# Optimization experiments

Hardware: AMD Instinct MI355X
Metric: run time of the kernel (lower is better)

Reference implementation:

```python
import jax, jax.numpy as jnp
import numpy as np

ITER_ROUTING = 3
FINAL_LAMBDA = 0.01
EPS = 1e-9

N = 4
CHILD_SPACE = 12
KERNEL = 3
STRIDE = 1
CHILD_CAPS = 16
PARENT_CAPS = 32
POSE = 16


def _routing_map(child_space, k, s):
    # (child_space^2, parent_space^2) binary map: child c feeds parent p.
    parent_space = (child_space - k) // s + 1
    m = np.zeros((child_space * child_space, parent_space * parent_space), np.float32)
    for pr in range(parent_space):
        for pc in range(parent_space):
            p = pr * parent_space + pc
            for r in range(k):
                for c in range(k):
                    m[(pr * s + r) * child_space + (pc * s + c), p] = 1.0
    return m


def setup_inputs() -> dict:
    key = jax.random.key(0)
    k1, k2, k3, k4 = jax.random.split(key, 4)
    parent_space = (CHILD_SPACE - KERNEL) // STRIDE + 1
    kk = KERNEL * KERNEL
    votes = jax.random.normal(k1, (N * parent_space * parent_space, kk * CHILD_CAPS, PARENT_CAPS, POSE), jnp.float32)
    acts = jax.random.uniform(k2, (N * parent_space * parent_space, kk * CHILD_CAPS, 1), dtype=jnp.float32)
    beta_v = jax.random.normal(k3, (1, 1, 1, 1, PARENT_CAPS, 1), jnp.float32)
    beta_a = jax.random.normal(k4, (1, 1, 1, 1, PARENT_CAPS, 1), jnp.float32)
    srm = jnp.asarray(_routing_map(CHILD_SPACE, KERNEL, STRIDE))
    return {"votes_ij": votes, "activations_i": acts, "beta_v": beta_v, "beta_a": beta_a,
            "spatial_routing_matrix": srm, "batch_size": N, "kk": kk}


def _em_routing(votes_ij, activations_i, beta_v, beta_a, srm, batch_size, kk):
    Nb = batch_size
    C2, P2 = srm.shape  # child_space^2, parent_space^2
    P = int(round(P2 ** 0.5))
    K_total, O, ch = votes_ij.shape[1], votes_ij.shape[2], votes_ij.shape[3]
    child_caps = K_total // kk

    votes = votes_ij.reshape(Nb, P, P, K_total, O, ch)
    act_i = activations_i.reshape(Nb, P, P, K_total, 1, 1)

    # children per parent, ascending child index (stable argsort on -1/0 values)
    cidx = jnp.argsort(-srm, axis=0)[:kk].T           # (P2, kk)
    seg = cidx.reshape(-1)                            # (P2*kk,) child id per (parent, slot)
    ppc = jnp.sum(srm, axis=1)                        # parents-per-child, (C2,)
    # init_rr: 1 / (parents_per_child * parent_caps + 1e-9), gathered per parent slot
    rr0 = (1.0 / (ppc[cidx] * O + 1e-9)).reshape(1, P, P, kk, 1, 1)
    rr = jnp.broadcast_to(rr0, (1, P, P, kk, child_caps, O)).reshape(1, P, P, K_total, O, 1)

    layer_norm_factor = 100.0 / (float(K_total) / float(O))

    def m_step(rr, it):
        lam = FINAL_LAMBDA * (1.0 - 0.95 ** (it + 1))
        rr_prime = rr * act_i                                            # (N,P,P,K,O,1)
        rr_prime_sum = jnp.sum(rr_prime, axis=-3, keepdims=True)         # (N,P,P,1,O,1)
        mean_j = jnp.sum(rr_prime * votes, axis=-3, keepdims=True) / (rr_prime_sum + EPS)
        var_j = jnp.sum(rr_prime * jnp.square(votes - mean_j), axis=-3, keepdims=True) / (rr_prime_sum + EPS)
        cost_j_h = (beta_v + 0.5 * jnp.log(var_j + EPS)) * rr_prime_sum * layer_norm_factor
        cost_j = jnp.sum(cost_j_h, axis=-1, keepdims=True)               # (N,P,P,1,O,1)
        cost_mean = jnp.mean(cost_j, axis=-2, keepdims=True)
        cost_stdv = jnp.sqrt(jnp.sum(jnp.square(cost_j - cost_mean), axis=-2, keepdims=True) / O)
        act_j = jax.nn.sigmoid(lam * (beta_a + (cost_mean - cost_j) / (cost_stdv + EPS)))
        return act_j, mean_j, var_j

    def e_step(act_j, mean_j, var_j):
        # log N(vote; mean_j, var_j) per parent + log activation
        o_p0 = -jnp.sum(jnp.square(votes - mean_j) / (2.0 * var_j), axis=-1, keepdims=True)
        o_p2 = -0.5 * jnp.sum(jnp.log(2.0 * np.pi * var_j), axis=-1, keepdims=True)
        zz = jnp.log(act_j + EPS) + o_p0 + o_p2                          # (N,P,P,K,O,1)
        # softmax over ALL parents of each child (spatial kk slots x parent_caps),
        # done via segment reductions keyed by child id (== sparse/softmax/dense of original)
        z = jnp.moveaxis(zz.reshape(Nb, P2 * kk, child_caps, O), 1, 0)   # (P2*kk, N, cc, O)
        m = jax.ops.segment_max(jnp.max(z, axis=-1), seg, num_segments=C2)  # (C2, N, cc)
        m = jnp.where(jnp.isinf(m), 0.0, m)
        e = jnp.exp(z - m[seg][..., None])
        denom = jax.ops.segment_sum(jnp.sum(e, axis=-1), seg, num_segments=C2)
        rr_new = e / denom[seg][..., None]
        return jnp.moveaxis(rr_new, 0, 1).reshape(Nb, P, P, K_total, O, 1)

    for it in range(ITER_ROUTING):
        act_j, mean_j, var_j = m_step(rr, it)
        if it < ITER_ROUTING - 1:
            rr = e_step(act_j, mean_j, var_j)

    poses_j = mean_j[:, :, :, 0]        # (N,P,P,O,16)
    activations_j = act_j[:, :, :, 0]   # (N,P,P,O,1)
    return poses_j, activations_j


def reference(votes_ij, activations_i, beta_v, beta_a, spatial_routing_matrix, batch_size, kk):
    return _em_routing(votes_ij, activations_i, beta_v, beta_a, spatial_routing_matrix, batch_size, kk)
```

## Files before the change

kernel.cpp:

```cpp
#include <hip/hip_runtime.h>
#include <hip/hip_fp16.h>
#include <math.h>

#define NB     4
#define P      10
#define P2     100
#define CS     12
#define CCAPS  16
#define KTOT   144
#define O      32
#define POSE   16
#define VSZ    73728
#define EPSF   1e-9f
#define LNF    22.2222222222222222f
#define TWO_PI 6.28318530717958647f
#define NBP    400
#define NKQ    3
#define KPU    48
#define SUNITS (NBP*NKQ)
#define EUNITS (NB*CS*CS*2)

#define LAM0 0.0005f
#define LAM1 0.000975f
#define LAM2 0.00142625f

__device__ float g_rr [NBP*KTOT*O];
__device__ float g_zz [NBP*KTOT*O];
__device__ float g_m1 [SUNITS*512];
__device__ float g_m2 [SUNITS*512];
__device__ float g_sv [SUNITS*O];

__device__ __forceinline__ int npar(int x) {
    int a = x + 1, b = CS - x;
    int m = a < 3 ? a : 3;
    return m < b ? m : b;
}

__device__ __forceinline__ void up8(uint4 u, float* f) {
    float2 a = __half22float2(*(__half2*)&u.x);
    float2 b = __half22float2(*(__half2*)&u.y);
    float2 c = __half22float2(*(__half2*)&u.z);
    float2 d = __half22float2(*(__half2*)&u.w);
    f[0] = a.x; f[1] = a.y; f[2] = b.x; f[3] = b.y;
    f[4] = c.x; f[5] = c.y; f[6] = d.x; f[7] = d.y;
}

__global__ __launch_bounds__(256)
void v_kernel(const float* __restrict__ votes, const float* __restrict__ acts,
              __half* __restrict__ hv)
{
    __shared__ float actl[KPU];
    __shared__ __align__(16) float rrp[KPU*O];
    __shared__ float4 lm1[256];
    __shared__ float4 lm2[256];
    __shared__ float  lss[256];

    const int tid = threadIdx.x;
    const int u   = blockIdx.x;
    const int bp  = u / NKQ;
    const int kq  = u - bp * NKQ;
    const int k0  = kq * KPU;
    const int ks  = tid >> 7;
    const int q   = tid & 127;
    const int o   = q >> 2;

    if (tid < KPU) actl[tid] = acts[bp * KTOT + k0 + tid];
    __syncthreads();

    for (int f = tid; f < KPU * O / 4; f += 256) {
        int kl = f >> 3;
        int kg = k0 + kl, kslot = kg >> 4;
        int kr = kslot / 3, kc = kslot - kr * 3;
        int p = bp % P2, pr = p / P, pc = p - pr * P;
        float ppc = (float)(npar(pr + kr) * npar(pc + kc));
        float r = actl[kl] / (ppc * 32.0f + EPSF);
        ((float4*)rrp)[f] = make_float4(r, r, r, r);
    }
    __syncthreads();

    const float* vb  = votes + (size_t)bp * VSZ + (size_t)(k0 + ks * 24) * 512 + q * 4;
    __half*      hb  = hv    + (size_t)bp * VSZ + (size_t)(k0 + ks * 24) * 512 + q * 4;
    const float* rr0 = rrp + (ks * 24) * O + o;
    float  s  = 0.f;
    float4 m1 = make_float4(0.f, 0.f, 0.f, 0.f);
    float4 m2 = make_float4(0.f, 0.f, 0.f, 0.f);
    #pragma unroll 8
    for (int i = 0; i < 24; ++i) {
        float  rp = rr0[i * O];
        float4 v  = *(const float4*)(vb + i * 512);
        s += rp;
        m1.x += rp * v.x;       m1.y += rp * v.y;
        m1.z += rp * v.z;       m1.w += rp * v.w;
        m2.x += rp * v.x * v.x; m2.y += rp * v.y * v.y;
        m2.z += rp * v.z * v.z; m2.w += rp * v.w * v.w;
        __half2 ha = __floats2half2_rn(v.x, v.y);
        __half2 hbv = __floats2half2_rn(v.z, v.w);
        uint2 st;
        st.x = *(unsigned int*)&ha;
        st.y = *(unsigned int*)&hbv;
        *(uint2*)(hb + i * 512) = st;
    }
    lm1[tid] = m1; lm2[tid] = m2; lss[tid] = s;
    __syncthreads();

    if (tid < 128) {
        float4 a = lm1[tid], b = lm1[tid + 128];
        m1 = make_float4(a.x + b.x, a.y + b.y, a.z + b.z, a.w + b.w);
        a = lm2[tid]; b = lm2[tid + 128];
        m2 = make_float4(a.x + b.x, a.y + b.y, a.z + b.z, a.w + b.w);
        s = lss[tid] + lss[tid + 128];
        ((float4*)g_m1)[u * 128 + tid] = m1;
        ((float4*)g_m2)[u * 128 + tid] = m2;
        if ((tid & 3) == 0) g_sv[u * O + (tid >> 2)] = s;
    }
}

__global__ __launch_bounds__(256)
void s16_kernel(const __half* __restrict__ hv, const float* __restrict__ acts)
{
    __shared__ float actl[KPU];
    __shared__ __align__(16) float rrp[KPU*O];
    __shared__ float4 lm1[512];
    __shared__ float4 lm2[512];
    __shared__ float  lss[256];

    const int tid = threadIdx.x;
    const int u   = blockIdx.x;
    const int bp  = u / NKQ;
    const int kq  = u - bp * NKQ;
    const int k0  = kq * KPU;
    const int ks  = tid >> 6;
    const int qp  = tid & 63;
    const int o   = qp >> 1;

    if (tid < KPU) actl[tid] = acts[bp * KTOT + k0 + tid];
    __syncthreads();

    for (int f = tid; f < KPU * O / 4; f += 256) {
        int kl = f >> 3;
        float4 r4 = ((const float4*)(g_rr + (size_t)bp * (KTOT * O) + k0 * O))[f];
        float a = actl[kl];
        r4.x *= a; r4.y *= a; r4.z *= a; r4.w *= a;
        ((float4*)rrp)[f] = r4;
    }
    __syncthreads();

    const __half* vb = hv + (size_t)bp * VSZ + (size_t)(k0 + ks * 12) * 512 + qp * 8;
    const float* rr0 = rrp + (ks * 12) * O + o;
    float s = 0.f;
    float m1[8], m2[8];
    #pragma unroll
    for (int j = 0; j < 8; ++j) { m1[j] = 0.f; m2[j] = 0.f; }
    #pragma unroll 4
    for (int i = 0; i < 12; ++i) {
        float rp = rr0[i * O];
        uint4 u4 = *(const uint4*)(vb + i * 512);
        float f[8]; up8(u4, f);
        s += rp;
        #pragma unroll
        for (int j = 0; j < 8; ++j) {
            m1[j] += rp * f[j];
            m2[j] += rp * f[j] * f[j];
        }
    }
    lm1[tid*2]   = make_float4(m1[0], m1[1], m1[2], m1[3]);
    lm1[tid*2+1] = make_float4(m1[4], m1[5], m1[6], m1[7]);
    lm2[tid*2]   = make_float4(m2[0], m2[1], m2[2], m2[3]);
    lm2[tid*2+1] = make_float4(m2[4], m2[5], m2[6], m2[7]);
    lss[tid] = s;
    __syncthreads();

    if (tid < 64) {
        #pragma unroll
        for (int j = 0; j < 2; ++j) {
            float4 a0 = lm1[(tid)*2+j],       a1 = lm1[(64+tid)*2+j];
            float4 a2 = lm1[(128+tid)*2+j],   a3 = lm1[(192+tid)*2+j];
            float4 r = make_float4(a0.x+a1.x+a2.x+a3.x, a0.y+a1.y+a2.y+a3.y,
                                   a0.z+a1.z+a2.z+a3.z, a0.w+a1.w+a2.w+a3.w);
            ((float4*)g_m1)[u * 128 + tid*2 + j] = r;
            float4 b0 = lm2[(tid)*2+j],       b1 = lm2[(64+tid)*2+j];
            float4 b2 = lm2[(128+tid)*2+j],   b3 = lm2[(192+tid)*2+j];
            float4 r2 = make_float4(b0.x+b1.x+b2.x+b3.x, b0.y+b1.y+b2.y+b3.y,
                                    b0.z+b1.z+b2.z+b3.z, b0.w+b1.w+b2.w+b3.w);
            ((float4*)g_m2)[u * 128 + tid*2 + j] = r2;
        }
        float sr = lss[tid] + lss[64+tid] + lss[128+tid] + lss[192+tid];
        if ((tid & 1) == 0) g_sv[u * O + (tid >> 1)] = sr;
    }
}

__device__ __forceinline__ void finish_bp(int bp, int tid, float lam,
                                          const float* __restrict__ beta_v,
                                          const float* __restrict__ beta_a,
                                          float4& mean, float4& i2,
                                          float& aj, float& lv2out,
                                          float* costl )
{
    const int o = tid >> 2, c4 = tid & 3;
    float4 m1 = make_float4(0.f, 0.f, 0.f, 0.f);
    float4 m2 = make_float4(0.f, 0.f, 0.f, 0.f);
    float  s  = 0.f;
    #pragma unroll
    for (int j = 0; j < NKQ; ++j) {
        float4 a = ((const float4*)g_m1)[(bp * NKQ + j) * 128 + tid];
        float4 b = ((const float4*)g_m2)[(bp * NKQ + j) * 128 + tid];
        m1.x += a.x; m1.y += a.y; m1.z += a.z; m1.w += a.w;
        m2.x += b.x; m2.y += b.y; m2.z += b.z; m2.w += b.w;
        s += g_sv[(bp * NKQ + j) * O + o];
    }
    float denom = s + EPSF;
    mean = make_float4(m1.x / denom, m1.y / denom, m1.z / denom, m1.w / denom);
    float4 var;
    var.x = fmaxf(m2.x / denom - mean.x * mean.x, 1e-30f);
    var.y = fmaxf(m2.y / denom - mean.y * mean.y, 1e-30f);
    var.z = fmaxf(m2.z / denom - mean.z * mean.z, 1e-30f);
    var.w = fmaxf(m2.w / denom - mean.w * mean.w, 1e-30f);
    i2 = make_float4(0.5f / var.x, 0.5f / var.y, 0.5f / var.z, 0.5f / var.w);
    float lve = logf(var.x + EPSF) + logf(var.y + EPSF)
              + logf(var.z + EPSF) + logf(var.w + EPSF);
    float lv2 = logf(TWO_PI * var.x) + logf(TWO_PI * var.y)
              + logf(TWO_PI * var.z) + logf(TWO_PI * var.w);
    lve += __shfl_xor(lve, 1); lve += __shfl_xor(lve, 2);
    lv2 += __shfl_xor(lv2, 1); lv2 += __shfl_xor(lv2, 2);
    lv2out = lv2;
    if (c4 == 0) costl[o] = (16.f * beta_v[o] + 0.5f * lve) * s * LNF;
    __syncthreads();
    float cm = 0.f;
    #pragma unroll
    for (int i = 0; i < O; ++i) cm += costl[i];
    cm *= (1.f / 32.f);
    float sq = 0.f;
    #pragma unroll
    for (int i = 0; i < O; ++i) { float d = costl[i] - cm; sq += d * d; }
    float cstd = sqrtf(sq * (1.f / 32.f));
    aj = 1.f / (1.f + expf(-lam * (beta_a[o] + (cm - costl[o]) / (cstd + EPSF))));
}

__global__ __launch_bounds__(256)
void zf16_kernel(const __half* __restrict__ hv,
                 const float* __restrict__ beta_v,
                 const float* __restrict__ beta_a, float lam)
{
    __shared__ float4 ml[128];
    __shared__ float4 il[128];
    __shared__ float  zl[O];
    __shared__ float  costl[O];
    __shared__ __align__(16) float zzl[KPU*O];

    const int tid = threadIdx.x;
    const int u   = blockIdx.x;
    const int bp  = u / NKQ;
    const int kq  = u - bp * NKQ;
    const int k0  = kq * KPU;
    const int ks  = tid >> 6;
    const int qp  = tid & 63;
    const int o   = qp >> 1;
    const int h   = qp & 1;

    {
        float4 mean, i2; float aj, lv2;
        if (tid < 128) {
            finish_bp(bp, tid, lam, beta_v, beta_a, mean, i2, aj, lv2, costl);
            ml[tid] = mean; il[tid] = i2;
            if ((tid & 3) == 0)
                zl[tid >> 2] = logf(aj + EPSF) - 0.5f * lv2;
        } else {
            __syncthreads();
        }
    }
    __syncthreads();

    const __half* vb = hv + (size_t)bp * VSZ + (size_t)(k0 + ks * 12) * 512 + qp * 8;
    float4 mA = ml[o*4 + h*2], mB = ml[o*4 + h*2 + 1];
    float4 iA = il[o*4 + h*2], iB = il[o*4 + h*2 + 1];
    float  zp = zl[o];
    #pragma unroll 4
    for (int i = 0; i < 12; ++i) {
        uint4 u4 = *(const uint4*)(vb + i * 512);
        float f[8]; up8(u4, f);
        float d0 = f[0]-mA.x, d1 = f[1]-mA.y, d2 = f[2]-mA.z, d3 = f[3]-mA.w;
        float d4 = f[4]-mB.x, d5 = f[5]-mB.y, d6 = f[6]-mB.z, d7 = f[7]-mB.w;
        float t = d0*d0*iA.x + d1*d1*iA.y + d2*d2*iA.z + d3*d3*iA.w
                + d4*d4*iB.x + d5*d5*iB.y + d6*d6*iB.z + d7*d7*iB.w;
        t += __shfl_xor(t, 1);
        if (h == 0) zzl[(ks * 12 + i) * O + o] = zp - t;
    }
    __syncthreads();
    float4* dst = (float4*)(g_zz + (size_t)bp * (KTOT * O) + k0 * O);
    for (int f = tid; f < KPU * O / 4; f += 256)
        dst[f] = ((float4*)zzl)[f];
}

__global__ __launch_bounds__(256)
void f_last_kernel(const float* __restrict__ beta_v,
                   const float* __restrict__ beta_a,
                   float* __restrict__ out, float lam)
{
    __shared__ float costl[O];
    const int tid = threadIdx.x;
    const int bp  = blockIdx.x;
    float4 mean, i2; float aj, lv2;
    if (tid < 128) {
        finish_bp(bp, tid, lam, beta_v, beta_a, mean, i2, aj, lv2, costl);
        ((float4*)out)[bp * 128 + tid] = mean;
        if ((tid & 3) == 0)
            out[(size_t)NBP * 512 + bp * O + (tid >> 2)] = aj;
    } else {
        __syncthreads();
    }
}

__global__ __launch_bounds__(256)
void e_kernel()
{
    const int tid = threadIdx.x;
    const int u   = blockIdx.x;
    const int b   = u / (CS * CS * 2);
    int r = u - b * (CS * CS * 2);
    const int child = r >> 1, half = r & 1;
    const int cr = child / CS, cl = child - cr * CS;
    const int cc = half * 8 + (tid >> 5), o = tid & 31;

    float zz[9];
    float vmax = -1e30f;
    #pragma unroll
    for (int kr = 0; kr < 3; ++kr) {
        int pr_ = cr - kr;
        #pragma unroll
        for (int kc = 0; kc < 3; ++kc) {
            int pc_ = cl - kc, si = kr * 3 + kc;
            float z = -1e30f;
            if (pr_ >= 0 && pr_ < P && pc_ >= 0 && pc_ < P) {
                int bpp = b * P2 + pr_ * P + pc_;
                z = g_zz[(size_t)bpp * (KTOT * O) + (si * CCAPS + cc) * O + o];
            }
            zz[si] = z;
            vmax = fmaxf(vmax, z);
        }
    }
    vmax = fmaxf(vmax, __shfl_xor(vmax, 1));
    vmax = fmaxf(vmax, __shfl_xor(vmax, 2));
    vmax = fmaxf(vmax, __shfl_xor(vmax, 4));
    vmax = fmaxf(vmax, __shfl_xor(vmax, 8));
    vmax = fmaxf(vmax, __shfl_xor(vmax, 16));

    float ps = 0.f;
    #pragma unroll
    for (int si = 0; si < 9; ++si) {
        float e = (zz[si] > -1e29f) ? expf(zz[si] - vmax) : 0.f;
        zz[si] = e;
        ps += e;
    }
    ps += __shfl_xor(ps, 1);
    ps += __shfl_xor(ps, 2);
    ps += __shfl_xor(ps, 4);
    ps += __shfl_xor(ps, 8);
    ps += __shfl_xor(ps, 16);
    float inv = 1.f / ps;

    #pragma unroll
    for (int kr = 0; kr < 3; ++kr) {
        int pr_ = cr - kr;
        #pragma unroll
        for (int kc = 0; kc < 3; ++kc) {
            int pc_ = cl - kc, si = kr * 3 + kc;
            if (pr_ >= 0 && pr_ < P && pc_ >= 0 && pc_ < P) {
                int bpp = b * P2 + pr_ * P + pc_;
                g_rr[(size_t)bpp * (KTOT * O) + (si * CCAPS + cc) * O + o] = zz[si] * inv;
            }
        }
    }
}

extern "C" void kernel_launch(void* const* d_in, const int* in_sizes, int n_in,
                              void* d_out, int out_size, void* d_ws, size_t ws_size,
                              hipStream_t stream)
{
    (void)in_sizes; (void)n_in; (void)out_size; (void)ws_size;

    const float* votes = (const float*)d_in[0];
    const float* acts  = (const float*)d_in[1];
    const float* bv    = (const float*)d_in[2];
    const float* ba    = (const float*)d_in[3];
    float* out = (float*)d_out;
    __half* hv = (__half*)d_ws;

    dim3 t(256);
    v_kernel<<<dim3(SUNITS), t, 0, stream>>>(votes, acts, hv);
    zf16_kernel<<<dim3(SUNITS), t, 0, stream>>>(hv, bv, ba, LAM0);
    e_kernel<<<dim3(EUNITS), t, 0, stream>>>();

    s16_kernel<<<dim3(SUNITS), t, 0, stream>>>(hv, acts);
    zf16_kernel<<<dim3(SUNITS), t, 0, stream>>>(hv, bv, ba, LAM1);
    e_kernel<<<dim3(EUNITS), t, 0, stream>>>();

    s16_kernel<<<dim3(SUNITS), t, 0, stream>>>(hv, acts);
    f_last_kernel<<<dim3(NBP), t, 0, stream>>>(bv, ba, out, LAM2);
}
```

Before: 257.5 us.

## Fuse softmax e-step into s16 m-step kernel and prefetch votes into registers

```diff
diff --git a/kernel.cpp b/kernel.cpp
--- a/kernel.cpp
+++ b/kernel.cpp
@@ -18,13 +18,11 @@
 #define NKQ    3
 #define KPU    48
 #define SUNITS (NBP*NKQ)
-#define EUNITS (NB*CS*CS*2)
 
 #define LAM0 0.0005f
 #define LAM1 0.000975f
 #define LAM2 0.00142625f
 
-__device__ float g_rr [NBP*KTOT*O];
 __device__ float g_zz [NBP*KTOT*O];
 __device__ float g_m1 [SUNITS*512];
 __device__ float g_m2 [SUNITS*512];
@@ -93,7 +91,7 @@
         m1.z += rp * v.z;       m1.w += rp * v.w;
         m2.x += rp * v.x * v.x; m2.y += rp * v.y * v.y;
         m2.z += rp * v.z * v.z; m2.w += rp * v.w * v.w;
-        __half2 ha = __floats2half2_rn(v.x, v.y);
+        __half2 ha  = __floats2half2_rn(v.x, v.y);
         __half2 hbv = __floats2half2_rn(v.z, v.w);
         uint2 st;
         st.x = *(unsigned int*)&ha;
@@ -115,14 +113,63 @@
     }
 }
 
+__device__ __forceinline__ void finish_bp(int bp, int tid, float lam,
+                                          const float* __restrict__ beta_v,
+                                          const float* __restrict__ beta_a,
+                                          float4& mean, float4& i2,
+                                          float& aj, float& lv2out,
+                                          float* costl )
+{
+    const int o = tid >> 2, c4 = tid & 3;
+    float4 m1 = make_float4(0.f, 0.f, 0.f, 0.f);
+    float4 m2 = make_float4(0.f, 0.f, 0.f, 0.f);
+    float  s  = 0.f;
+    #pragma unroll
+    for (int j = 0; j < NKQ; ++j) {
+        float4 a = ((const float4*)g_m1)[(bp * NKQ + j) * 128 + tid];
+        float4 b = ((const float4*)g_m2)[(bp * NKQ + j) * 128 + tid];
+        m1.x += a.x; m1.y += a.y; m1.z += a.z; m1.w += a.w;
+        m2.x += b.x; m2.y += b.y; m2.z += b.z; m2.w += b.w;
+        s += g_sv[(bp * NKQ + j) * O + o];
+    }
+    float denom = s + EPSF;
+    mean = make_float4(m1.x / denom, m1.y / denom, m1.z / denom, m1.w / denom);
+    float4 var;
+    var.x = fmaxf(m2.x / denom - mean.x * mean.x, 1e-30f);
+    var.y = fmaxf(m2.y / denom - mean.y * mean.y, 1e-30f);
+    var.z = fmaxf(m2.z / denom - mean.z * mean.z, 1e-30f);
+    var.w = fmaxf(m2.w / denom - mean.w * mean.w, 1e-30f);
+    i2 = make_float4(0.5f / var.x, 0.5f / var.y, 0.5f / var.z, 0.5f / var.w);
+    float lve = logf(var.x + EPSF) + logf(var.y + EPSF)
+              + logf(var.z + EPSF) + logf(var.w + EPSF);
+    float lv2 = logf(TWO_PI * var.x) + logf(TWO_PI * var.y)
+              + logf(TWO_PI * var.z) + logf(TWO_PI * var.w);
+    lve += __shfl_xor(lve, 1); lve += __shfl_xor(lve, 2);
+    lv2 += __shfl_xor(lv2, 1); lv2 += __shfl_xor(lv2, 2);
+    lv2out = lv2;
+    if (c4 == 0) costl[o] = (16.f * beta_v[o] + 0.5f * lve) * s * LNF;
+    __syncthreads();
+    float cm = 0.f;
+    #pragma unroll
+    for (int i = 0; i < O; ++i) cm += costl[i];
+    cm *= (1.f / 32.f);
+    float sq = 0.f;
+    #pragma unroll
+    for (int i = 0; i < O; ++i) { float d = costl[i] - cm; sq += d * d; }
+    float cstd = sqrtf(sq * (1.f / 32.f));
+    aj = 1.f / (1.f + expf(-lam * (beta_a[o] + (cm - costl[o]) / (cstd + EPSF))));
+}
+
 __global__ __launch_bounds__(256)
-void s16_kernel(const __half* __restrict__ hv, const float* __restrict__ acts)
-{
-    __shared__ float actl[KPU];
-    __shared__ __align__(16) float rrp[KPU*O];
-    __shared__ float4 lm1[512];
-    __shared__ float4 lm2[512];
-    __shared__ float  lss[256];
+void zf16_kernel(const __half* __restrict__ hv,
+                 const float* __restrict__ beta_v,
+                 const float* __restrict__ beta_a, float lam)
+{
+    __shared__ float4 ml[128];
+    __shared__ float4 il[128];
+    __shared__ float  zl[O];
+    __shared__ float  costl[O];
+    __shared__ __align__(16) float zzl[KPU*O];
 
     const int tid = threadIdx.x;
     const int u   = blockIdx.x;
@@ -132,30 +179,127 @@
     const int ks  = tid >> 6;
     const int qp  = tid & 63;
     const int o   = qp >> 1;
-
-    if (tid < KPU) actl[tid] = acts[bp * KTOT + k0 + tid];
-    __syncthreads();
-
-    for (int f = tid; f < KPU * O / 4; f += 256) {
-        int kl = f >> 3;
-        float4 r4 = ((const float4*)(g_rr + (size_t)bp * (KTOT * O) + k0 * O))[f];
-        float a = actl[kl];
-        r4.x *= a; r4.y *= a; r4.z *= a; r4.w *= a;
-        ((float4*)rrp)[f] = r4;
-    }
-    __syncthreads();
+    const int h   = qp & 1;
 
     const __half* vb = hv + (size_t)bp * VSZ + (size_t)(k0 + ks * 12) * 512 + qp * 8;
-    const float* rr0 = rrp + (ks * 12) * O + o;
+    uint4 vv[12];
+    #pragma unroll
+    for (int i = 0; i < 12; ++i) vv[i] = *(const uint4*)(vb + i * 512);
+
+    {
+        float4 mean, i2; float aj, lv2;
+        if (tid < 128) {
+            finish_bp(bp, tid, lam, beta_v, beta_a, mean, i2, aj, lv2, costl);
+            ml[tid] = mean; il[tid] = i2;
+            if ((tid & 3) == 0)
+                zl[tid >> 2] = logf(aj + EPSF) - 0.5f * lv2;
+        } else {
+            __syncthreads();
+        }
+    }
+    __syncthreads();
+
+    float4 mA = ml[o*4 + h*2], mB = ml[o*4 + h*2 + 1];
+    float4 iA = il[o*4 + h*2], iB = il[o*4 + h*2 + 1];
+    float  zp = zl[o];
+    #pragma unroll
+    for (int i = 0; i < 12; ++i) {
+        float f[8]; up8(vv[i], f);
+        float d0 = f[0]-mA.x, d1 = f[1]-mA.y, d2 = f[2]-mA.z, d3 = f[3]-mA.w;
+        float d4 = f[4]-mB.x, d5 = f[5]-mB.y, d6 = f[6]-mB.z, d7 = f[7]-mB.w;
+        float t = d0*d0*iA.x + d1*d1*iA.y + d2*d2*iA.z + d3*d3*iA.w
+                + d4*d4*iB.x + d5*d5*iB.y + d6*d6*iB.z + d7*d7*iB.w;
+        t += __shfl_xor(t, 1);
+        if (h == 0) zzl[(ks * 12 + i) * O + o] = zp - t;
+    }
+    __syncthreads();
+    float4* dst = (float4*)(g_zz + (size_t)bp * (KTOT * O) + k0 * O);
+    for (int f = tid; f < KPU * O / 4; f += 256)
+        dst[f] = ((float4*)zzl)[f];
+}
+
+__global__ __launch_bounds__(256)
+void se16_kernel(const __half* __restrict__ hv, const float* __restrict__ acts)
+{
+    __shared__ __align__(16) float rrp[KPU*O];
+    __shared__ float4 lm1[512];
+    __shared__ float4 lm2[512];
+    __shared__ float  lss[256];
+
+    const int tid = threadIdx.x;
+    const int u   = blockIdx.x;
+    const int bp  = u / NKQ;
+    const int kq  = u - bp * NKQ;
+    const int k0  = kq * KPU;
+    const int p   = bp % P2;
+    const int b   = bp / P2;
+    const int pr  = p / P, pc = p - pr * P;
+
+    const int ks  = tid >> 6;
+    const int qp  = tid & 63;
+    const int o_s = qp >> 1;
+
+    const __half* vb = hv + (size_t)bp * VSZ + (size_t)(k0 + ks * 12) * 512 + qp * 8;
+    uint4 vv[12];
+    #pragma unroll
+    for (int i = 0; i < 12; ++i) vv[i] = *(const uint4*)(vb + i * 512);
+
+    const int ccl = tid >> 5;
+    const int o   = tid & 31;
+    const int cr  = pr + kq;
+
+    #pragma unroll
+    for (int ci = 0; ci < 3; ++ci) {
+        const int cl = pc + ci;
+        #pragma unroll
+        for (int ccp = 0; ccp < 2; ++ccp) {
+            const int cc = ccl + 8 * ccp;
+            float zv[9];
+            float vmax = -1e30f;
+            #pragma unroll
+            for (int sip = 0; sip < 9; ++sip) {
+                const int krp = sip / 3, kcp = sip - krp * 3;
+                const int pr2 = cr - krp, pc2 = cl - kcp;
+                float z = -1e30f;
+                if (pr2 >= 0 && pr2 < P && pc2 >= 0 && pc2 < P) {
+                    const int bp2 = b * P2 + pr2 * P + pc2;
+                    z = g_zz[(size_t)bp2 * (KTOT * O) + (sip * CCAPS + cc) * O + o];
+                }
+                zv[sip] = z;
+                vmax = fmaxf(vmax, z);
+            }
+            vmax = fmaxf(vmax, __shfl_xor(vmax, 1));
+            vmax = fmaxf(vmax, __shfl_xor(vmax, 2));
+            vmax = fmaxf(vmax, __shfl_xor(vmax, 4));
+            vmax = fmaxf(vmax, __shfl_xor(vmax, 8));
+            vmax = fmaxf(vmax, __shfl_xor(vmax, 16));
+            float ps = 0.f;
+            #pragma unroll
+            for (int sip = 0; sip < 9; ++sip)
+                ps += (zv[sip] > -1e29f) ? expf(zv[sip] - vmax) : 0.f;
+            ps += __shfl_xor(ps, 1);
+            ps += __shfl_xor(ps, 2);
+            ps += __shfl_xor(ps, 4);
+            ps += __shfl_xor(ps, 8);
+            ps += __shfl_xor(ps, 16);
+            const float inv = 1.f / ps;
+            const int si = 3 * kq + ci;
+            const float av = acts[bp * KTOT + si * CCAPS + cc];
+            const float rp = expf(zv[si] - vmax) * inv * av;
+            rrp[(ci * CCAPS + cc) * O + o] = rp;
+        }
+    }
+    __syncthreads();
+
+    const float* rr0 = rrp + (ks * 12) * O + o_s;
     float s = 0.f;
     float m1[8], m2[8];
     #pragma unroll
     for (int j = 0; j < 8; ++j) { m1[j] = 0.f; m2[j] = 0.f; }
-    #pragma unroll 4
+    #pragma unroll
     for (int i = 0; i < 12; ++i) {
         float rp = rr0[i * O];
-        uint4 u4 = *(const uint4*)(vb + i * 512);
-        float f[8]; up8(u4, f);
+        float f[8]; up8(vv[i], f);
         s += rp;
         #pragma unroll
         for (int j = 0; j < 8; ++j) {
@@ -189,108 +333,6 @@
     }
 }
 
-__device__ __forceinline__ void finish_bp(int bp, int tid, float lam,
-                                          const float* __restrict__ beta_v,
-                                          const float* __restrict__ beta_a,
-                                          float4& mean, float4& i2,
-                                          float& aj, float& lv2out,
-                                          float* costl )
-{
-    const int o = tid >> 2, c4 = tid & 3;
-    float4 m1 = make_float4(0.f, 0.f, 0.f, 0.f);
-    float4 m2 = make_float4(0.f, 0.f, 0.f, 0.f);
-    float  s  = 0.f;
-    #pragma unroll
-    for (int j = 0; j < NKQ; ++j) {
-        float4 a = ((const float4*)g_m1)[(bp * NKQ + j) * 128 + tid];
-        float4 b = ((const float4*)g_m2)[(bp * NKQ + j) * 128 + tid];
-        m1.x += a.x; m1.y += a.y; m1.z += a.z; m1.w += a.w;
-        m2.x += b.x; m2.y += b.y; m2.z += b.z; m2.w += b.w;
-        s += g_sv[(bp * NKQ + j) * O + o];
-    }
-    float denom = s + EPSF;
-    mean = make_float4(m1.x / denom, m1.y / denom, m1.z / denom, m1.w / denom);
-    float4 var;
-    var.x = fmaxf(m2.x / denom - mean.x * mean.x, 1e-30f);
-    var.y = fmaxf(m2.y / denom - mean.y * mean.y, 1e-30f);
-    var.z = fmaxf(m2.z / denom - mean.z * mean.z, 1e-30f);
-    var.w = fmaxf(m2.w / denom - mean.w * mean.w, 1e-30f);
-    i2 = make_float4(0.5f / var.x, 0.5f / var.y, 0.5f / var.z, 0.5f / var.w);
-    float lve = logf(var.x + EPSF) + logf(var.y + EPSF)
-              + logf(var.z + EPSF) + logf(var.w + EPSF);
-    float lv2 = logf(TWO_PI * var.x) + logf(TWO_PI * var.y)
-              + logf(TWO_PI * var.z) + logf(TWO_PI * var.w);
-    lve += __shfl_xor(lve, 1); lve += __shfl_xor(lve, 2);
-    lv2 += __shfl_xor(lv2, 1); lv2 += __shfl_xor(lv2, 2);
-    lv2out = lv2;
-    if (c4 == 0) costl[o] = (16.f * beta_v[o] + 0.5f * lve) * s * LNF;
-    __syncthreads();
-    float cm = 0.f;
-    #pragma unroll
-    for (int i = 0; i < O; ++i) cm += costl[i];
-    cm *= (1.f / 32.f);
-    float sq = 0.f;
-    #pragma unroll
-    for (int i = 0; i < O; ++i) { float d = costl[i] - cm; sq += d * d; }
-    float cstd = sqrtf(sq * (1.f / 32.f));
-    aj = 1.f / (1.f + expf(-lam * (beta_a[o] + (cm - costl[o]) / (cstd + EPSF))));
-}
-
-__global__ __launch_bounds__(256)
-void zf16_kernel(const __half* __restrict__ hv,
-                 const float* __restrict__ beta_v,
-                 const float* __restrict__ beta_a, float lam)
-{
-    __shared__ float4 ml[128];
-    __shared__ float4 il[128];
-    __shared__ float  zl[O];
-    __shared__ float  costl[O];
-    __shared__ __align__(16) float zzl[KPU*O];
-
-    const int tid = threadIdx.x;
-    const int u   = blockIdx.x;
-    const int bp  = u / NKQ;
-    const int kq  = u - bp * NKQ;
-    const int k0  = kq * KPU;
-    const int ks  = tid >> 6;
-    const int qp  = tid & 63;
-    const int o   = qp >> 1;
-    const int h   = qp & 1;
-
-    {
-        float4 mean, i2; float aj, lv2;
-        if (tid < 128) {
-            finish_bp(bp, tid, lam, beta_v, beta_a, mean, i2, aj, lv2, costl);
-            ml[tid] = mean; il[tid] = i2;
-            if ((tid & 3) == 0)
-                zl[tid >> 2] = logf(aj + EPSF) - 0.5f * lv2;
-        } else {
-            __syncthreads();
-        }
-    }
-    __syncthreads();
-
-    const __half* vb = hv + (size_t)bp * VSZ + (size_t)(k0 + ks * 12) * 512 + qp * 8;
-    float4 mA = ml[o*4 + h*2], mB = ml[o*4 + h*2 + 1];
-    float4 iA = il[o*4 + h*2], iB = il[o*4 + h*2 + 1];
-    float  zp = zl[o];
-    #pragma unroll 4
-    for (int i = 0; i < 12; ++i) {
-        uint4 u4 = *(const uint4*)(vb + i * 512);
-        float f[8]; up8(u4, f);
-        float d0 = f[0]-mA.x, d1 = f[1]-mA.y, d2 = f[2]-mA.z, d3 = f[3]-mA.w;
-        float d4 = f[4]-mB.x, d5 = f[5]-mB.y, d6 = f[6]-mB.z, d7 = f[7]-mB.w;
-        float t = d0*d0*iA.x + d1*d1*iA.y + d2*d2*iA.z + d3*d3*iA.w
-                + d4*d4*iB.x + d5*d5*iB.y + d6*d6*iB.z + d7*d7*iB.w;
-        t += __shfl_xor(t, 1);
-        if (h == 0) zzl[(ks * 12 + i) * O + o] = zp - t;
-    }
-    __syncthreads();
-    float4* dst = (float4*)(g_zz + (size_t)bp * (KTOT * O) + k0 * O);
-    for (int f = tid; f < KPU * O / 4; f += 256)
-        dst[f] = ((float4*)zzl)[f];
-}
-
 __global__ __launch_bounds__(256)
 void f_last_kernel(const float* __restrict__ beta_v,
                    const float* __restrict__ beta_a,
@@ -310,68 +352,6 @@
     }
 }
 
-__global__ __launch_bounds__(256)
-void e_kernel()
-{
-    const int tid = threadIdx.x;
-    const int u   = blockIdx.x;
-    const int b   = u / (CS * CS * 2);
-    int r = u - b * (CS * CS * 2);
-    const int child = r >> 1, half = r & 1;
-    const int cr = child / CS, cl = child - cr * CS;
-    const int cc = half * 8 + (tid >> 5), o = tid & 31;
-
-    float zz[9];
-    float vmax = -1e30f;
-    #pragma unroll
-    for (int kr = 0; kr < 3; ++kr) {
-        int pr_ = cr - kr;
-        #pragma unroll
-        for (int kc = 0; kc < 3; ++kc) {
-            int pc_ = cl - kc, si = kr * 3 + kc;
-            float z = -1e30f;
-            if (pr_ >= 0 && pr_ < P && pc_ >= 0 && pc_ < P) {
-                int bpp = b * P2 + pr_ * P + pc_;
-                z = g_zz[(size_t)bpp * (KTOT * O) + (si * CCAPS + cc) * O + o];
-            }
-            zz[si] = z;
-            vmax = fmaxf(vmax, z);
-        }
-    }
-    vmax = fmaxf(vmax, __shfl_xor(vmax, 1));
-    vmax = fmaxf(vmax, __shfl_xor(vmax, 2));
-    vmax = fmaxf(vmax, __shfl_xor(vmax, 4));
-    vmax = fmaxf(vmax, __shfl_xor(vmax, 8));
-    vmax = fmaxf(vmax, __shfl_xor(vmax, 16));
-
-    float ps = 0.f;
-    #pragma unroll
-    for (int si = 0; si < 9; ++si) {
-        float e = (zz[si] > -1e29f) ? expf(zz[si] - vmax) : 0.f;
-        zz[si] = e;
-        ps += e;
-    }
-    ps += __shfl_xor(ps, 1);
-    ps += __shfl_xor(ps, 2);
-    ps += __shfl_xor(ps, 4);
-    ps += __shfl_xor(ps, 8);
-    ps += __shfl_xor(ps, 16);
-    float inv = 1.f / ps;
-
-    #pragma unroll
-    for (int kr = 0; kr < 3; ++kr) {
-        int pr_ = cr - kr;
-        #pragma unroll
-        for (int kc = 0; kc < 3; ++kc) {
-            int pc_ = cl - kc, si = kr * 3 + kc;
-            if (pr_ >= 0 && pr_ < P && pc_ >= 0 && pc_ < P) {
-                int bpp = b * P2 + pr_ * P + pc_;
-                g_rr[(size_t)bpp * (KTOT * O) + (si * CCAPS + cc) * O + o] = zz[si] * inv;
-            }
-        }
-    }
-}
-
 extern "C" void kernel_launch(void* const* d_in, const int* in_sizes, int n_in,
                               void* d_out, int out_size, void* d_ws, size_t ws_size,
                               hipStream_t stream)
@@ -388,12 +368,8 @@
     dim3 t(256);
     v_kernel<<<dim3(SUNITS), t, 0, stream>>>(votes, acts, hv);
     zf16_kernel<<<dim3(SUNITS), t, 0, stream>>>(hv, bv, ba, LAM0);
-    e_kernel<<<dim3(EUNITS), t, 0, stream>>>();
-
-    s16_kernel<<<dim3(SUNITS), t, 0, stream>>>(hv, acts);
+    se16_kernel<<<dim3(SUNITS), t, 0, stream>>>(hv, acts);
     zf16_kernel<<<dim3(SUNITS), t, 0, stream>>>(hv, bv, ba, LAM1);
-    e_kernel<<<dim3(EUNITS), t, 0, stream>>>();
-
-    s16_kernel<<<dim3(SUNITS), t, 0, stream>>>(hv, acts);
+    se16_kernel<<<dim3(SUNITS), t, 0, stream>>>(hv, acts);
     f_last_kernel<<<dim3(NBP), t, 0, stream>>>(bv, ba, out, LAM2);
 }
```

Measured after the change: 286.7 us. 11.3% more time.

## Fuse M-step statistics with finish and z computation in one block per parent

Applied to the files above, without the earlier changes.

```diff
diff --git a/kernel.cpp b/kernel.cpp
--- a/kernel.cpp
+++ b/kernel.cpp
@@ -15,20 +15,14 @@
 #define LNF    22.2222222222222222f
 #define TWO_PI 6.28318530717958647f
 #define NBP    400
-#define NKQ    3
-#define KPU    48
-#define SUNITS (NBP*NKQ)
 #define EUNITS (NB*CS*CS*2)
 
 #define LAM0 0.0005f
 #define LAM1 0.000975f
 #define LAM2 0.00142625f
 
-__device__ float g_rr [NBP*KTOT*O];
 __device__ float g_zz [NBP*KTOT*O];
-__device__ float g_m1 [SUNITS*512];
-__device__ float g_m2 [SUNITS*512];
-__device__ float g_sv [SUNITS*O];
+__device__ float g_rrp[NBP*KTOT*O];
 
 __device__ __forceinline__ int npar(int x) {
     int a = x + 1, b = CS - x;
@@ -45,55 +39,54 @@
     f[4] = c.x; f[5] = c.y; f[6] = d.x; f[7] = d.y;
 }
 
-__global__ __launch_bounds__(256)
-void v_kernel(const float* __restrict__ votes, const float* __restrict__ acts,
-              __half* __restrict__ hv)
+__global__ __launch_bounds__(512)
+void v400_kernel(const float* __restrict__ votes, const float* __restrict__ acts,
+                 __half* __restrict__ hv,
+                 const float* __restrict__ beta_v, const float* __restrict__ beta_a,
+                 float lam)
 {
-    __shared__ float actl[KPU];
-    __shared__ __align__(16) float rrp[KPU*O];
-    __shared__ float4 lm1[256];
-    __shared__ float4 lm2[256];
-    __shared__ float  lss[256];
+    __shared__ float  rr1[KTOT];
+    __shared__ float4 lm1[512];
+    __shared__ float4 lm2[512];
+    __shared__ float  lss[512];
+    __shared__ float4 ml[128];
+    __shared__ float4 il[128];
+    __shared__ float  zl[O];
+    __shared__ float  costl[O];
+    __shared__ __align__(16) float zzl[KTOT*O];
 
     const int tid = threadIdx.x;
-    const int u   = blockIdx.x;
-    const int bp  = u / NKQ;
-    const int kq  = u - bp * NKQ;
-    const int k0  = kq * KPU;
+    const int bp  = blockIdx.x;
+    const int p   = bp % P2;
+    const int pr  = p / P, pc = p - pr * P;
     const int ks  = tid >> 7;
     const int q   = tid & 127;
     const int o   = q >> 2;
-
-    if (tid < KPU) actl[tid] = acts[bp * KTOT + k0 + tid];
-    __syncthreads();
-
-    for (int f = tid; f < KPU * O / 4; f += 256) {
-        int kl = f >> 3;
-        int kg = k0 + kl, kslot = kg >> 4;
+    const int c4  = q & 3;
+
+    if (tid < KTOT) {
+        int kslot = tid >> 4;
         int kr = kslot / 3, kc = kslot - kr * 3;
-        int p = bp % P2, pr = p / P, pc = p - pr * P;
         float ppc = (float)(npar(pr + kr) * npar(pc + kc));
-        float r = actl[kl] / (ppc * 32.0f + EPSF);
-        ((float4*)rrp)[f] = make_float4(r, r, r, r);
-    }
-    __syncthreads();
-
-    const float* vb  = votes + (size_t)bp * VSZ + (size_t)(k0 + ks * 24) * 512 + q * 4;
-    __half*      hb  = hv    + (size_t)bp * VSZ + (size_t)(k0 + ks * 24) * 512 + q * 4;
-    const float* rr0 = rrp + (ks * 24) * O + o;
+        rr1[tid] = acts[bp * KTOT + tid] / (ppc * 32.0f + EPSF);
+    }
+    __syncthreads();
+
+    const float* vb = votes + (size_t)bp * VSZ + (size_t)(ks * 36) * 512 + q * 4;
+    __half*      hb = hv    + (size_t)bp * VSZ + (size_t)(ks * 36) * 512 + q * 4;
     float  s  = 0.f;
     float4 m1 = make_float4(0.f, 0.f, 0.f, 0.f);
     float4 m2 = make_float4(0.f, 0.f, 0.f, 0.f);
-    #pragma unroll 8
-    for (int i = 0; i < 24; ++i) {
-        float  rp = rr0[i * O];
+    #pragma unroll 6
+    for (int i = 0; i < 36; ++i) {
+        float  rp = rr1[ks * 36 + i];
         float4 v  = *(const float4*)(vb + i * 512);
         s += rp;
         m1.x += rp * v.x;       m1.y += rp * v.y;
         m1.z += rp * v.z;       m1.w += rp * v.w;
         m2.x += rp * v.x * v.x; m2.y += rp * v.y * v.y;
         m2.z += rp * v.z * v.z; m2.w += rp * v.w * v.w;
-        __half2 ha = __floats2half2_rn(v.x, v.y);
+        __half2 ha  = __floats2half2_rn(v.x, v.y);
         __half2 hbv = __floats2half2_rn(v.z, v.w);
         uint2 st;
         st.x = *(unsigned int*)&ha;
@@ -103,57 +96,108 @@
     lm1[tid] = m1; lm2[tid] = m2; lss[tid] = s;
     __syncthreads();
 
+    float lv2 = 0.f, cost_o = 0.f;
     if (tid < 128) {
-        float4 a = lm1[tid], b = lm1[tid + 128];
+        float4 a, b;
+        a = lm1[tid];       b = lm1[128 + tid];
         m1 = make_float4(a.x + b.x, a.y + b.y, a.z + b.z, a.w + b.w);
-        a = lm2[tid]; b = lm2[tid + 128];
+        a = lm1[256 + tid]; b = lm1[384 + tid];
+        m1.x += a.x + b.x; m1.y += a.y + b.y; m1.z += a.z + b.z; m1.w += a.w + b.w;
+        a = lm2[tid];       b = lm2[128 + tid];
         m2 = make_float4(a.x + b.x, a.y + b.y, a.z + b.z, a.w + b.w);
-        s = lss[tid] + lss[tid + 128];
-        ((float4*)g_m1)[u * 128 + tid] = m1;
-        ((float4*)g_m2)[u * 128 + tid] = m2;
-        if ((tid & 3) == 0) g_sv[u * O + (tid >> 2)] = s;
-    }
-}
-
-__global__ __launch_bounds__(256)
-void s16_kernel(const __half* __restrict__ hv, const float* __restrict__ acts)
+        a = lm2[256 + tid]; b = lm2[384 + tid];
+        m2.x += a.x + b.x; m2.y += a.y + b.y; m2.z += a.z + b.z; m2.w += a.w + b.w;
+        s = lss[tid] + lss[128 + tid] + lss[256 + tid] + lss[384 + tid];
+
+        float denom = s + EPSF;
+        float4 mean = make_float4(m1.x/denom, m1.y/denom, m1.z/denom, m1.w/denom);
+        float4 var;
+        var.x = fmaxf(m2.x/denom - mean.x*mean.x, 1e-30f);
+        var.y = fmaxf(m2.y/denom - mean.y*mean.y, 1e-30f);
+        var.z = fmaxf(m2.z/denom - mean.z*mean.z, 1e-30f);
+        var.w = fmaxf(m2.w/denom - mean.w*mean.w, 1e-30f);
+        float4 i2 = make_float4(0.5f/var.x, 0.5f/var.y, 0.5f/var.z, 0.5f/var.w);
+        ml[tid] = mean; il[tid] = i2;
+        float lve = logf(var.x+EPSF)+logf(var.y+EPSF)+logf(var.z+EPSF)+logf(var.w+EPSF);
+        float l2  = logf(TWO_PI*var.x)+logf(TWO_PI*var.y)+logf(TWO_PI*var.z)+logf(TWO_PI*var.w);
+        lve += __shfl_xor(lve, 1); lve += __shfl_xor(lve, 2);
+        l2  += __shfl_xor(l2, 1);  l2  += __shfl_xor(l2, 2);
+        lv2 = l2;
+        cost_o = (16.f * beta_v[o] + 0.5f * lve) * s * LNF;
+        if (c4 == 0) costl[o] = cost_o;
+    }
+    __syncthreads();
+    if (tid < 128) {
+        float cm = 0.f;
+        #pragma unroll
+        for (int i = 0; i < O; ++i) cm += costl[i];
+        cm *= (1.f / 32.f);
+        float sq = 0.f;
+        #pragma unroll
+        for (int i = 0; i < O; ++i) { float d = costl[i] - cm; sq += d * d; }
+        float cstd = sqrtf(sq * (1.f / 32.f));
+        float aj = 1.f / (1.f + expf(-lam * (beta_a[o] + (cm - cost_o) / (cstd + EPSF))));
+        if (c4 == 0) zl[o] = logf(aj + EPSF) - 0.5f * lv2;
+    }
+    __syncthreads();
+
+    {
+        float4 mean = ml[q];
+        float4 iv   = il[q];
+        float  zp   = zl[o];
+        #pragma unroll 6
+        for (int i = 0; i < 36; ++i) {
+            float4 v = *(const float4*)(vb + i * 512);
+            float dx = v.x - mean.x, dy = v.y - mean.y;
+            float dz = v.z - mean.z, dw = v.w - mean.w;
+            float t = dx*dx*iv.x + dy*dy*iv.y + dz*dz*iv.z + dw*dw*iv.w;
+            t += __shfl_xor(t, 1); t += __shfl_xor(t, 2);
+            if (c4 == 0) zzl[(ks * 36 + i) * O + o] = zp - t;
+        }
+    }
+    __syncthreads();
+    float4* dst = (float4*)(g_zz + (size_t)bp * (KTOT * O));
+    for (int f = tid; f < KTOT * O / 4; f += 512)
+        dst[f] = ((float4*)zzl)[f];
+}
+
+template<bool LAST>
+__global__ __launch_bounds__(512)
+void m16_kernel(const __half* __restrict__ hv,
+                const float* __restrict__ beta_v, const float* __restrict__ beta_a,
+                float* __restrict__ out, float lam)
 {
-    __shared__ float actl[KPU];
-    __shared__ __align__(16) float rrp[KPU*O];
-    __shared__ float4 lm1[512];
-    __shared__ float4 lm2[512];
-    __shared__ float  lss[256];
+    __shared__ __align__(16) float rrp[KTOT*O];
+    __shared__ float4 lm1[1024];
+    __shared__ float4 lm2[1024];
+    __shared__ float  lss[512];
+    __shared__ float4 rm1[128];
+    __shared__ float4 rm2[128];
+    __shared__ float  rsq[64];
+    __shared__ float4 ml[128];
+    __shared__ float4 il[128];
+    __shared__ float  zl[O];
+    __shared__ float  costl[O];
 
     const int tid = threadIdx.x;
-    const int u   = blockIdx.x;
-    const int bp  = u / NKQ;
-    const int kq  = u - bp * NKQ;
-    const int k0  = kq * KPU;
+    const int bp  = blockIdx.x;
     const int ks  = tid >> 6;
     const int qp  = tid & 63;
     const int o   = qp >> 1;
-
-    if (tid < KPU) actl[tid] = acts[bp * KTOT + k0 + tid];
-    __syncthreads();
-
-    for (int f = tid; f < KPU * O / 4; f += 256) {
-        int kl = f >> 3;
-        float4 r4 = ((const float4*)(g_rr + (size_t)bp * (KTOT * O) + k0 * O))[f];
-        float a = actl[kl];
-        r4.x *= a; r4.y *= a; r4.z *= a; r4.w *= a;
-        ((float4*)rrp)[f] = r4;
-    }
-    __syncthreads();
-
-    const __half* vb = hv + (size_t)bp * VSZ + (size_t)(k0 + ks * 12) * 512 + qp * 8;
-    const float* rr0 = rrp + (ks * 12) * O + o;
+    const int h   = qp & 1;
+
+    for (int f = tid; f < KTOT * O / 4; f += 512)
+        ((float4*)rrp)[f] = ((const float4*)(g_rrp + (size_t)bp * (KTOT * O)))[f];
+    __syncthreads();
+
+    const __half* vb = hv + (size_t)bp * VSZ + (size_t)(ks * 18) * 512 + qp * 8;
     float s = 0.f;
     float m1[8], m2[8];
     #pragma unroll
     for (int j = 0; j < 8; ++j) { m1[j] = 0.f; m2[j] = 0.f; }
-    #pragma unroll 4
-    for (int i = 0; i < 12; ++i) {
-        float rp = rr0[i * O];
+    #pragma unroll 6
+    for (int i = 0; i < 18; ++i) {
+        float rp = rrp[(ks * 18 + i) * O + o];
         uint4 u4 = *(const uint4*)(vb + i * 512);
         float f[8]; up8(u4, f);
         s += rp;
@@ -173,145 +217,92 @@
     if (tid < 64) {
         #pragma unroll
         for (int j = 0; j < 2; ++j) {
-            float4 a0 = lm1[(tid)*2+j],       a1 = lm1[(64+tid)*2+j];
-            float4 a2 = lm1[(128+tid)*2+j],   a3 = lm1[(192+tid)*2+j];
-            float4 r = make_float4(a0.x+a1.x+a2.x+a3.x, a0.y+a1.y+a2.y+a3.y,
-                                   a0.z+a1.z+a2.z+a3.z, a0.w+a1.w+a2.w+a3.w);
-            ((float4*)g_m1)[u * 128 + tid*2 + j] = r;
-            float4 b0 = lm2[(tid)*2+j],       b1 = lm2[(64+tid)*2+j];
-            float4 b2 = lm2[(128+tid)*2+j],   b3 = lm2[(192+tid)*2+j];
-            float4 r2 = make_float4(b0.x+b1.x+b2.x+b3.x, b0.y+b1.y+b2.y+b3.y,
-                                    b0.z+b1.z+b2.z+b3.z, b0.w+b1.w+b2.w+b3.w);
-            ((float4*)g_m2)[u * 128 + tid*2 + j] = r2;
-        }
-        float sr = lss[tid] + lss[64+tid] + lss[128+tid] + lss[192+tid];
-        if ((tid & 1) == 0) g_sv[u * O + (tid >> 1)] = sr;
-    }
-}
-
-__device__ __forceinline__ void finish_bp(int bp, int tid, float lam,
-                                          const float* __restrict__ beta_v,
-                                          const float* __restrict__ beta_a,
-                                          float4& mean, float4& i2,
-                                          float& aj, float& lv2out,
-                                          float* costl )
-{
-    const int o = tid >> 2, c4 = tid & 3;
-    float4 m1 = make_float4(0.f, 0.f, 0.f, 0.f);
-    float4 m2 = make_float4(0.f, 0.f, 0.f, 0.f);
-    float  s  = 0.f;
-    #pragma unroll
-    for (int j = 0; j < NKQ; ++j) {
-        float4 a = ((const float4*)g_m1)[(bp * NKQ + j) * 128 + tid];
-        float4 b = ((const float4*)g_m2)[(bp * NKQ + j) * 128 + tid];
-        m1.x += a.x; m1.y += a.y; m1.z += a.z; m1.w += a.w;
-        m2.x += b.x; m2.y += b.y; m2.z += b.z; m2.w += b.w;
-        s += g_sv[(bp * NKQ + j) * O + o];
-    }
-    float denom = s + EPSF;
-    mean = make_float4(m1.x / denom, m1.y / denom, m1.z / denom, m1.w / denom);
-    float4 var;
-    var.x = fmaxf(m2.x / denom - mean.x * mean.x, 1e-30f);
-    var.y = fmaxf(m2.y / denom - mean.y * mean.y, 1e-30f);
-    var.z = fmaxf(m2.z / denom - mean.z * mean.z, 1e-30f);
-    var.w = fmaxf(m2.w / denom - mean.w * mean.w, 1e-30f);
-    i2 = make_float4(0.5f / var.x, 0.5f / var.y, 0.5f / var.z, 0.5f / var.w);
-    float lve = logf(var.x + EPSF) + logf(var.y + EPSF)
-              + logf(var.z + EPSF) + logf(var.w + EPSF);
-    float lv2 = logf(TWO_PI * var.x) + logf(TWO_PI * var.y)
-              + logf(TWO_PI * var.z) + logf(TWO_PI * var.w);
-    lve += __shfl_xor(lve, 1); lve += __shfl_xor(lve, 2);
-    lv2 += __shfl_xor(lv2, 1); lv2 += __shfl_xor(lv2, 2);
-    lv2out = lv2;
-    if (c4 == 0) costl[o] = (16.f * beta_v[o] + 0.5f * lve) * s * LNF;
-    __syncthreads();
-    float cm = 0.f;
-    #pragma unroll
-    for (int i = 0; i < O; ++i) cm += costl[i];
-    cm *= (1.f / 32.f);
-    float sq = 0.f;
-    #pragma unroll
-    for (int i = 0; i < O; ++i) { float d = costl[i] - cm; sq += d * d; }
-    float cstd = sqrtf(sq * (1.f / 32.f));
-    aj = 1.f / (1.f + expf(-lam * (beta_a[o] + (cm - costl[o]) / (cstd + EPSF))));
+            float4 a = lm1[tid*2+j];
+            float4 bq = lm2[tid*2+j];
+            #pragma unroll
+            for (int w = 1; w < 8; ++w) {
+                float4 x = lm1[(w*64+tid)*2+j];
+                float4 y = lm2[(w*64+tid)*2+j];
+                a.x += x.x; a.y += x.y; a.z += x.z; a.w += x.w;
+                bq.x += y.x; bq.y += y.y; bq.z += y.z; bq.w += y.w;
+            }
+            rm1[tid*2+j] = a;
+            rm2[tid*2+j] = bq;
+        }
+        float sr = 0.f;
+        #pragma unroll
+        for (int w = 0; w < 8; ++w) sr += lss[w*64+tid];
+        rsq[tid] = sr;
+    }
+    __syncthreads();
+
+    float lv2 = 0.f, cost_o = 0.f;
+    const int of = tid >> 2, c4 = tid & 3;
+    if (tid < 128) {
+        float4 fm1 = rm1[tid], fm2 = rm2[tid];
+        float  fs  = rsq[of * 2];
+        float denom = fs + EPSF;
+        float4 mean = make_float4(fm1.x/denom, fm1.y/denom, fm1.z/denom, fm1.w/denom);
+        float4 var;
+        var.x = fmaxf(fm2.x/denom - mean.x*mean.x, 1e-30f);
+        var.y = fmaxf(fm2.y/denom - mean.y*mean.y, 1e-30f);
+        var.z = fmaxf(fm2.z/denom - mean.z*mean.z, 1e-30f);
+        var.w = fmaxf(fm2.w/denom - mean.w*mean.w, 1e-30f);
+        float4 i2 = make_float4(0.5f/var.x, 0.5f/var.y, 0.5f/var.z, 0.5f/var.w);
+        ml[tid] = mean; il[tid] = i2;
+        float lve = logf(var.x+EPSF)+logf(var.y+EPSF)+logf(var.z+EPSF)+logf(var.w+EPSF);
+        float l2  = logf(TWO_PI*var.x)+logf(TWO_PI*var.y)+logf(TWO_PI*var.z)+logf(TWO_PI*var.w);
+        lve += __shfl_xor(lve, 1); lve += __shfl_xor(lve, 2);
+        l2  += __shfl_xor(l2, 1);  l2  += __shfl_xor(l2, 2);
+        lv2 = l2;
+        cost_o = (16.f * beta_v[of] + 0.5f * lve) * fs * LNF;
+        if (c4 == 0) costl[of] = cost_o;
+    }
+    __syncthreads();
+    if (tid < 128) {
+        float cm = 0.f;
+        #pragma unroll
+        for (int i = 0; i < O; ++i) cm += costl[i];
+        cm *= (1.f / 32.f);
+        float sq = 0.f;
+        #pragma unroll
+        for (int i = 0; i < O; ++i) { float d = costl[i] - cm; sq += d * d; }
+        float cstd = sqrtf(sq * (1.f / 32.f));
+        float aj = 1.f / (1.f + expf(-lam * (beta_a[of] + (cm - cost_o) / (cstd + EPSF))));
+        if (LAST) {
+            ((float4*)out)[bp * 128 + tid] = ml[tid];
+            if (c4 == 0) out[(size_t)NBP * 512 + bp * O + of] = aj;
+        } else {
+            if (c4 == 0) zl[of] = logf(aj + EPSF) - 0.5f * lv2;
+        }
+    }
+    if (LAST) return;
+    __syncthreads();
+
+    {
+        float4 mA = ml[o*4 + h*2], mB = ml[o*4 + h*2 + 1];
+        float4 iA = il[o*4 + h*2], iB = il[o*4 + h*2 + 1];
+        float  zp = zl[o];
+        #pragma unroll 6
+        for (int i = 0; i < 18; ++i) {
+            uint4 u4 = *(const uint4*)(vb + i * 512);
+            float f[8]; up8(u4, f);
+            float d0 = f[0]-mA.x, d1 = f[1]-mA.y, d2 = f[2]-mA.z, d3 = f[3]-mA.w;
+            float d4 = f[4]-mB.x, d5 = f[5]-mB.y, d6 = f[6]-mB.z, d7 = f[7]-mB.w;
+            float t = d0*d0*iA.x + d1*d1*iA.y + d2*d2*iA.z + d3*d3*iA.w
+                    + d4*d4*iB.x + d5*d5*iB.y + d6*d6*iB.z + d7*d7*iB.w;
+            t += __shfl_xor(t, 1);
+            if (h == 0) rrp[(ks * 18 + i) * O + o] = zp - t;
+        }
+    }
+    __syncthreads();
+    float4* dst = (float4*)(g_zz + (size_t)bp * (KTOT * O));
+    for (int f = tid; f < KTOT * O / 4; f += 512)
+        dst[f] = ((float4*)rrp)[f];
 }
 
 __global__ __launch_bounds__(256)
-void zf16_kernel(const __half* __restrict__ hv,
-                 const float* __restrict__ beta_v,
-                 const float* __restrict__ beta_a, float lam)
-{
-    __shared__ float4 ml[128];
-    __shared__ float4 il[128];
-    __shared__ float  zl[O];
-    __shared__ float  costl[O];
-    __shared__ __align__(16) float zzl[KPU*O];
-
-    const int tid = threadIdx.x;
-    const int u   = blockIdx.x;
-    const int bp  = u / NKQ;
-    const int kq  = u - bp * NKQ;
-    const int k0  = kq * KPU;
-    const int ks  = tid >> 6;
-    const int qp  = tid & 63;
-    const int o   = qp >> 1;
-    const int h   = qp & 1;
-
-    {
-        float4 mean, i2; float aj, lv2;
-        if (tid < 128) {
-            finish_bp(bp, tid, lam, beta_v, beta_a, mean, i2, aj, lv2, costl);
-            ml[tid] = mean; il[tid] = i2;
-            if ((tid & 3) == 0)
-                zl[tid >> 2] = logf(aj + EPSF) - 0.5f * lv2;
-        } else {
-            __syncthreads();
-        }
-    }
-    __syncthreads();
-
-    const __half* vb = hv + (size_t)bp * VSZ + (size_t)(k0 + ks * 12) * 512 + qp * 8;
-    float4 mA = ml[o*4 + h*2], mB = ml[o*4 + h*2 + 1];
-    float4 iA = il[o*4 + h*2], iB = il[o*4 + h*2 + 1];
-    float  zp = zl[o];
-    #pragma unroll 4
-    for (int i = 0; i < 12; ++i) {
-        uint4 u4 = *(const uint4*)(vb + i * 512);
-        float f[8]; up8(u4, f);
-        float d0 = f[0]-mA.x, d1 = f[1]-mA.y, d2 = f[2]-mA.z, d3 = f[3]-mA.w;
-        float d4 = f[4]-mB.x, d5 = f[5]-mB.y, d6 = f[6]-mB.z, d7 = f[7]-mB.w;
-        float t = d0*d0*iA.x + d1*d1*iA.y + d2*d2*iA.z + d3*d3*iA.w
-                + d4*d4*iB.x + d5*d5*iB.y + d6*d6*iB.z + d7*d7*iB.w;
-        t += __shfl_xor(t, 1);
-        if (h == 0) zzl[(ks * 12 + i) * O + o] = zp - t;
-    }
-    __syncthreads();
-    float4* dst = (float4*)(g_zz + (size_t)bp * (KTOT * O) + k0 * O);
-    for (int f = tid; f < KPU * O / 4; f += 256)
-        dst[f] = ((float4*)zzl)[f];
-}
-
-__global__ __launch_bounds__(256)
-void f_last_kernel(const float* __restrict__ beta_v,
-                   const float* __restrict__ beta_a,
-                   float* __restrict__ out, float lam)
-{
-    __shared__ float costl[O];
-    const int tid = threadIdx.x;
-    const int bp  = blockIdx.x;
-    float4 mean, i2; float aj, lv2;
-    if (tid < 128) {
-        finish_bp(bp, tid, lam, beta_v, beta_a, mean, i2, aj, lv2, costl);
-        ((float4*)out)[bp * 128 + tid] = mean;
-        if ((tid & 3) == 0)
-            out[(size_t)NBP * 512 + bp * O + (tid >> 2)] = aj;
-    } else {
-        __syncthreads();
-    }
-}
-
-__global__ __launch_bounds__(256)
-void e_kernel()
+void e_kernel(const float* __restrict__ acts)
 {
     const int tid = threadIdx.x;
     const int u   = blockIdx.x;
@@ -366,7 +357,9 @@
             int pc_ = cl - kc, si = kr * 3 + kc;
             if (pr_ >= 0 && pr_ < P && pc_ >= 0 && pc_ < P) {
                 int bpp = b * P2 + pr_ * P + pc_;
-                g_rr[(size_t)bpp * (KTOT * O) + (si * CCAPS + cc) * O + o] = zz[si] * inv;
+                float av = acts[bpp * KTOT + si * CCAPS + cc];
+                g_rrp[(size_t)bpp * (KTOT * O) + (si * CCAPS + cc) * O + o]
+                    = zz[si] * inv * av;
             }
         }
     }
@@ -385,15 +378,9 @@
     float* out = (float*)d_out;
     __half* hv = (__half*)d_ws;
 
-    dim3 t(256);
-    v_kernel<<<dim3(SUNITS), t, 0, stream>>>(votes, acts, hv);
-    zf16_kernel<<<dim3(SUNITS), t, 0, stream>>>(hv, bv, ba, LAM0);
-    e_kernel<<<dim3(EUNITS), t, 0, stream>>>();
-
-    s16_kernel<<<dim3(SUNITS), t, 0, stream>>>(hv, acts);
-    zf16_kernel<<<dim3(SUNITS), t, 0, stream>>>(hv, bv, ba, LAM1);
-    e_kernel<<<dim3(EUNITS), t, 0, stream>>>();
-
-    s16_kernel<<<dim3(SUNITS), t, 0, stream>>>(hv, acts);
-    f_last_kernel<<<dim3(NBP), t, 0, stream>>>(bv, ba, out, LAM2);
-}
+    v400_kernel<<<dim3(NBP), dim3(512), 0, stream>>>(votes, acts, hv, bv, ba, LAM0);
+    e_kernel<<<dim3(EUNITS), dim3(256), 0, stream>>>(acts);
+    m16_kernel<false><<<dim3(NBP), dim3(512), 0, stream>>>(hv, bv, ba, out, LAM1);
+    e_kernel<<<dim3(EUNITS), dim3(256), 0, stream>>>(acts);
+    m16_kernel<true ><<<dim3(NBP), dim3(512), 0, stream>>>(hv, bv, ba, out, LAM2);
+}
```

Measured after the change: 257.3 us. No clear change (-0.1%).
